# Optimization experiments

Measured on AMD Instinct MI355X. Metric: run time of the kernel, lower is better.

The kernel has to match this reference:

```python
import jax, jax.numpy as jnp
import numpy as np

DIM = 256
NUM_HEADS = 8
WH, WW = 7, 7
N = WH * WW
HEAD_DIM = DIM // NUM_HEADS
SCALE = HEAD_DIM ** -0.5
B_ = 4096
NW = 64  # windows per image


def _relative_position_index():
    # Swin relative position index: (N, N) int32 in [0, (2Wh-1)*(2Ww-1))
    coords = np.stack(np.meshgrid(np.arange(WH), np.arange(WW), indexing='ij'))  # (2, Wh, Ww)
    cf = coords.reshape(2, -1)  # (2, N)
    rel = cf[:, :, None] - cf[:, None, :]  # (2, N, N)
    rel = rel.transpose(1, 2, 0).copy()
    rel[:, :, 0] += WH - 1
    rel[:, :, 1] += WW - 1
    rel[:, :, 0] *= 2 * WW - 1
    return jnp.asarray(rel.sum(-1), dtype=jnp.int32)  # (N, N)


def setup_inputs() -> dict:
    key = jax.random.key(0)
    ks = jax.random.split(key, 7)
    x = jax.random.normal(ks[0], (B_, N, DIM), dtype=jnp.float32)
    mask = jax.random.normal(ks[1], (NW, N, N), dtype=jnp.float32)
    qkv_w = jax.random.normal(ks[2], (3 * DIM, DIM), dtype=jnp.float32) * 0.02
    qkv_b = jnp.zeros((3 * DIM,), dtype=jnp.float32)
    proj_w = jax.random.normal(ks[3], (DIM, DIM), dtype=jnp.float32) * 0.02
    proj_b = jnp.zeros((DIM,), dtype=jnp.float32)
    bias_table = jax.random.normal(ks[4], ((2 * WH - 1) * (2 * WW - 1), NUM_HEADS), dtype=jnp.float32) * 0.02
    rel_index = _relative_position_index()
    return {"x": x, "mask": mask, "qkv_w": qkv_w, "qkv_b": qkv_b,
            "proj_w": proj_w, "proj_b": proj_b, "bias_table": bias_table,
            "rel_index": rel_index}


def reference(x, mask, qkv_w, qkv_b, proj_w, proj_b, bias_table, rel_index):
    Bw, n, c = x.shape
    # qkv projection: (B_, N, 3C) -> (3, B_, nH, N, hd)
    qkv = (x @ qkv_w.T + qkv_b).reshape(Bw, n, 3, NUM_HEADS, HEAD_DIM)
    qkv = qkv.transpose(2, 0, 3, 1, 4)
    q, k, v = qkv[0], qkv[1], qkv[2]
    attn = jnp.einsum('bhqd,bhkd->bhqk', q * SCALE, k)  # (B_, nH, N, N)
    # gathered relative position bias: (nH, N, N)
    rpb = bias_table[rel_index.reshape(-1)].reshape(n, n, NUM_HEADS).transpose(2, 0, 1)
    attn = attn + rpb[None]
    # window mask: reshape batch into (B, nW) and broadcast mask per-window
    nW = mask.shape[0]
    attn = attn.reshape(Bw // nW, nW, NUM_HEADS, n, n) + mask[None, :, None]
    attn = attn.reshape(Bw, NUM_HEADS, n, n)
    attn = jax.nn.softmax(attn, axis=-1)
    out = jnp.einsum('bhqk,bhkd->bhqd', attn, v)  # (B_, nH, N, hd)
    out = out.transpose(0, 2, 1, 3).reshape(Bw, n, c)
    return out @ proj_w.T + proj_b
```

## Files before the change

kernel.cpp:

```cpp
#include <hip/hip_runtime.h>
#include <hip/hip_bf16.h>

typedef __bf16 bf16;
typedef __bf16 bf16x4v __attribute__((ext_vector_type(4)));
typedef __bf16 bf16x8 __attribute__((ext_vector_type(8)));
typedef float  f32x4  __attribute__((ext_vector_type(4)));
typedef float  f32x8  __attribute__((ext_vector_type(8)));

#define MFMA16(A,B,C) __builtin_amdgcn_mfma_f32_16x16x32_bf16((A),(B),(C),0,0,0)

constexpr int   N_TOK = 49;
constexpr int   DIM_C = 256;
constexpr float SCALE = 0.17677669529663687f;

constexpr int SMEM_ELEMS = N_TOK * 256;

constexpr size_t CB_BYTES    = 64ull * 8 * 64 * 64 * 4;
constexpr int    QKVW_ELEMS  = 768 * 256;
constexpr int    PROJW_ELEMS = 256 * 256;

__global__ __launch_bounds__(256) void build_cb_kernel(
    const float* __restrict__ bias_table, const float* __restrict__ mask,
    const int* __restrict__ rel_index, float* __restrict__ cb) {
  int idx = blockIdx.x * 256 + threadIdx.x;
  int j = idx & 63, m = (idx >> 6) & 63, h = (idx >> 12) & 7, w = idx >> 15;
  float v = 0.f;
  if (j < N_TOK && m < N_TOK)
    v = bias_table[rel_index[m * 49 + j] * 8 + h] + mask[(w * 49 + m) * 49 + j];
  cb[idx] = v;
}

__global__ __launch_bounds__(256) void cvt_w_kernel(
    const float* __restrict__ qkv_w, const float* __restrict__ proj_w,
    bf16* __restrict__ qkv_wb, bf16* __restrict__ proj_wb) {
  int i = blockIdx.x * 256 + threadIdx.x;
  if (i < QKVW_ELEMS) qkv_wb[i] = (bf16)qkv_w[i];
  else                proj_wb[i - QKVW_ELEMS] = (bf16)proj_w[i - QKVW_ELEMS];
}

__device__ __forceinline__ bf16x8 repack8(f32x4 Ta, f32x4 Tb, int l15, int lgp) {
  const int s0 = l15 + ((lgp & 1) << 5);
  const bool hi = (lgp & 2) != 0;
  bf16x8 F;
#pragma unroll
  for (int r = 0; r < 4; ++r) {
    float a0 = __shfl(Ta[r], s0);
    float b0 = __shfl(Tb[r], s0);
    F[r] = (bf16)(hi ? b0 : a0);
    float a1 = __shfl(Ta[r], s0 + 16);
    float b1 = __shfl(Tb[r], s0 + 16);
    F[r + 4] = (bf16)(hi ? b1 : a1);
  }
  return F;
}

__device__ __forceinline__ bf16x8 tile_read(const bf16* sm, int mt, int l15, int kk) {
  int m = mt * 16 + l15;
  int mc = m < N_TOK ? m : 48;
  return *reinterpret_cast<const bf16x8*>(&sm[mc * 256 + (kk ^ ((mc & 7) << 3))]);
}

__global__ __launch_bounds__(512, 4) void win_attn_kernel(
    const float* __restrict__ x, const bf16* __restrict__ qkv_wb,
    const float* __restrict__ qkv_b, const bf16* __restrict__ proj_wb,
    const float* __restrict__ proj_b, const float* __restrict__ cb,
    float* __restrict__ out) {
  __shared__ bf16 smem[SMEM_ELEMS];

  const int beta  = blockIdx.x;
  const int w_idx = beta >> 6;
  const int img   = beta & 63;
  const int b     = img * 64 + w_idx;
  const int tid   = threadIdx.x;
  const int wv    = tid >> 6;
  const int l     = tid & 63;
  const int l15   = l & 15, lgp = l >> 4;
  const int h     = wv;

  const f32x4 fzero = {0.f, 0.f, 0.f, 0.f};

  const float* xg = x + (size_t)b * (N_TOK * DIM_C);
  for (int c = tid; c < (N_TOK * DIM_C / 8); c += 512) {
    int m = c >> 5, k0 = (c & 31) * 8;
    f32x8 f = *reinterpret_cast<const f32x8*>(xg + m * 256 + k0);
    bf16x8 v;
#pragma unroll
    for (int e = 0; e < 8; ++e) v[e] = (bf16)f[e];
    *reinterpret_cast<bf16x8*>(&smem[m * 256 + (k0 ^ ((m & 7) << 3))]) = v;
  }
  __syncthreads();

  bf16x8 Qf[4], Kf[4];
  {
    f32x4 dq[2][4], dk[2][4];
#pragma unroll
    for (int i = 0; i < 2; ++i)
      for (int mt = 0; mt < 4; ++mt) { dq[i][mt] = fzero; dk[i][mt] = fzero; }
#pragma unroll 2
    for (int k0 = 0; k0 < 8; ++k0) {
      const int kk = k0 * 32 + lgp * 8;
      bf16x8 X[4];
#pragma unroll
      for (int mt = 0; mt < 4; ++mt) X[mt] = tile_read(smem, mt, l15, kk);
#pragma unroll
      for (int i = 0; i < 2; ++i) {
        int cq = (2 * h + i) * 16 + l15;
        bf16x8 Aq = *reinterpret_cast<const bf16x8*>(qkv_wb + cq * DIM_C + kk);
#pragma unroll
        for (int mt = 0; mt < 4; ++mt) dq[i][mt] = MFMA16(Aq, X[mt], dq[i][mt]);
        int ck = (16 + 2 * h + i) * 16 + l15;
        bf16x8 Ak = *reinterpret_cast<const bf16x8*>(qkv_wb + ck * DIM_C + kk);
#pragma unroll
        for (int mt = 0; mt < 4; ++mt) dk[i][mt] = MFMA16(Ak, X[mt], dk[i][mt]);
      }
    }
#pragma unroll
    for (int i = 0; i < 2; ++i) {
      f32x4 qb = *reinterpret_cast<const f32x4*>(qkv_b + (2 * h + i) * 16 + lgp * 4);
      f32x4 kb = *reinterpret_cast<const f32x4*>(qkv_b + 256 + (2 * h + i) * 16 + lgp * 4);
#pragma unroll
      for (int mt = 0; mt < 4; ++mt)
#pragma unroll
        for (int r = 0; r < 4; ++r) {
          dq[i][mt][r] = (dq[i][mt][r] + qb[r]) * SCALE;
          dk[i][mt][r] += kb[r];
        }
    }
#pragma unroll
    for (int mt = 0; mt < 4; ++mt) Qf[mt] = repack8(dq[0][mt], dq[1][mt], l15, lgp);
#pragma unroll
    for (int jt = 0; jt < 4; ++jt) Kf[jt] = repack8(dk[0][jt], dk[1][jt], l15, lgp);
  }

  bf16x8 Vf[2][2];
  {
    f32x4 dv[2][4];
#pragma unroll
    for (int i = 0; i < 2; ++i)
      for (int mt = 0; mt < 4; ++mt) dv[i][mt] = fzero;
#pragma unroll 2
    for (int k0 = 0; k0 < 8; ++k0) {
      const int kk = k0 * 32 + lgp * 8;
      bf16x8 X[4];
#pragma unroll
      for (int mt = 0; mt < 4; ++mt) X[mt] = tile_read(smem, mt, l15, kk);
#pragma unroll
      for (int i = 0; i < 2; ++i) {
        int cv = (32 + 2 * h + i) * 16 + l15;
        bf16x8 Bw = *reinterpret_cast<const bf16x8*>(qkv_wb + cv * DIM_C + kk);
#pragma unroll
        for (int mt = 0; mt < 4; ++mt) dv[i][mt] = MFMA16(X[mt], Bw, dv[i][mt]);
      }
    }
    __syncthreads();
#pragma unroll
    for (int i = 0; i < 2; ++i) {
      float vb = qkv_b[512 + (32 + 2 * h + i) * 16 + l15 - 512];
#pragma unroll
      for (int mt = 0; mt < 4; ++mt)
#pragma unroll
        for (int r = 0; r < 4; ++r) dv[i][mt][r] += vb;
#pragma unroll
      for (int ks = 0; ks < 2; ++ks)
        Vf[i][ks] = repack8(dv[i][ks * 2], dv[i][ks * 2 + 1], l15, lgp);
    }
  }

  const float* cbp = cb + ((size_t)(w_idx * 8 + h)) * 4096;
#pragma unroll
  for (int mt = 0; mt < 4; ++mt) {
    int mrow = mt * 16 + l15;
    f32x4 cb4[4];
#pragma unroll
    for (int jt = 0; jt < 4; ++jt)
      cb4[jt] = *reinterpret_cast<const f32x4*>(cbp + mrow * 64 + jt * 16 + lgp * 4);
    f32x4 e4[4];
#pragma unroll
    for (int jt = 0; jt < 4; ++jt) e4[jt] = MFMA16(Kf[jt], Qf[mt], fzero);
#pragma unroll
    for (int jt = 0; jt < 4; ++jt)
#pragma unroll
      for (int r = 0; r < 4; ++r) {
        float v = e4[jt][r] + cb4[jt][r];
        if (jt == 3) {
          if (r != 0 || lgp != 0) v = -3.0e38f;
        }
        e4[jt][r] = v;
      }
    float mx = e4[0][0];
#pragma unroll
    for (int jt = 0; jt < 4; ++jt)
#pragma unroll
      for (int r = 0; r < 4; ++r) mx = fmaxf(mx, e4[jt][r]);
    mx = fmaxf(mx, __shfl_xor(mx, 16));
    mx = fmaxf(mx, __shfl_xor(mx, 32));
    float sum = 0.f;
#pragma unroll
    for (int jt = 0; jt < 4; ++jt)
#pragma unroll
      for (int r = 0; r < 4; ++r) {
        float ex = __expf(e4[jt][r] - mx);
        e4[jt][r] = ex;
        sum += ex;
      }
    sum += __shfl_xor(sum, 16);
    sum += __shfl_xor(sum, 32);
    float rinv = 1.0f / sum;

    bf16x8 Pf0 = repack8(e4[0], e4[1], l15, lgp);
    bf16x8 Pf1 = repack8(e4[2], e4[3], l15, lgp);
    f32x4 pv0 = MFMA16(Vf[0][0], Pf0, fzero);
    pv0 = MFMA16(Vf[0][1], Pf1, pv0);
    f32x4 pv1 = MFMA16(Vf[1][0], Pf0, fzero);
    pv1 = MFMA16(Vf[1][1], Pf1, pv1);

    if (mrow < N_TOK) {
      bf16x4v w0, w1;
#pragma unroll
      for (int r = 0; r < 4; ++r) {
        w0[r] = (bf16)(pv0[r] * rinv);
        w1[r] = (bf16)(pv1[r] * rinv);
      }
      int sw = (mrow & 7) << 3;
      int c0 = 32 * h + lgp * 4;
      *reinterpret_cast<bf16x4v*>(&smem[mrow * 256 + (c0 ^ sw)]) = w0;
      *reinterpret_cast<bf16x4v*>(&smem[mrow * 256 + ((c0 + 16) ^ sw)]) = w1;
    }
  }
  __syncthreads();

  f32x4 acc2[2][4];
#pragma unroll
  for (int ci = 0; ci < 2; ++ci)
    for (int mt = 0; mt < 4; ++mt) acc2[ci][mt] = fzero;
#pragma unroll 2
  for (int k0 = 0; k0 < 8; ++k0) {
    const int kk = k0 * 32 + lgp * 8;
    bf16x8 Bao[4];
#pragma unroll
    for (int mt = 0; mt < 4; ++mt) Bao[mt] = tile_read(smem, mt, l15, kk);
#pragma unroll
    for (int ci = 0; ci < 2; ++ci) {
      int c = (2 * wv + ci) * 16 + l15;
      bf16x8 Aw = *reinterpret_cast<const bf16x8*>(proj_wb + c * DIM_C + kk);
#pragma unroll
      for (int mt = 0; mt < 4; ++mt) acc2[ci][mt] = MFMA16(Aw, Bao[mt], acc2[ci][mt]);
    }
  }
  float* ob = out + (size_t)b * (N_TOK * DIM_C);
#pragma unroll
  for (int ci = 0; ci < 2; ++ci) {
    int c0 = (2 * wv + ci) * 16 + lgp * 4;
    f32x4 pb = *reinterpret_cast<const f32x4*>(proj_b + c0);
#pragma unroll
    for (int mt = 0; mt < 4; ++mt) {
      int mrow = mt * 16 + l15;
      if (mrow < N_TOK) {
        f32x4 o;
#pragma unroll
        for (int r = 0; r < 4; ++r) o[r] = acc2[ci][mt][r] + pb[r];
        *reinterpret_cast<f32x4*>(ob + mrow * 256 + c0) = o;
      }
    }
  }
}

extern "C" void kernel_launch(void* const* d_in, const int* in_sizes, int n_in,
                              void* d_out, int out_size, void* d_ws, size_t ws_size,
                              hipStream_t stream) {
  const float* x          = (const float*)d_in[0];
  const float* mask       = (const float*)d_in[1];
  const float* qkv_w      = (const float*)d_in[2];
  const float* qkv_b      = (const float*)d_in[3];
  const float* proj_w     = (const float*)d_in[4];
  const float* proj_b     = (const float*)d_in[5];
  const float* bias_table = (const float*)d_in[6];
  const int*   rel_index  = (const int*)d_in[7];

  float* cb      = (float*)d_ws;
  bf16*  qkv_wb  = (bf16*)((char*)d_ws + CB_BYTES);
  bf16*  proj_wb = (bf16*)((char*)d_ws + CB_BYTES + QKVW_ELEMS * 2);

  hipLaunchKernelGGL(build_cb_kernel, dim3(8192), dim3(256), 0, stream,
                     bias_table, mask, rel_index, cb);
  hipLaunchKernelGGL(cvt_w_kernel, dim3(1024), dim3(256), 0, stream,
                     qkv_w, proj_w, qkv_wb, proj_wb);
  hipLaunchKernelGGL(win_attn_kernel, dim3(4096), dim3(512), 0, stream,
                     x, qkv_wb, qkv_b, proj_wb, proj_b, cb, (float*)d_out);
}
```

Before: 511.2 us.

## Split fused window attention into QKV GEMM, attention, and projection GEMM kernels

Replaces the single fused per-window kernel with three kernels: a tiled 128x128 QKV GEMM over all tokens that writes bf16 Q/K/V to workspace in head-major layout, a per-(window,head) attention kernel, and a tiled projection GEMM. The goal is better weight reuse and MFMA utilization from large GEMM tiles than the per-window fused version, which re-read weights for each window. In exchange it adds large intermediate round trips through global memory (Q/K/V and attention output, on the order of a hundred MB each way) and two extra launches, plus scattered 2-byte stores in the QKV epilogue.

After: 435.4 us. 14.8% less time.

```diff
diff --git a/kernel.cpp b/kernel.cpp
--- a/kernel.cpp
+++ b/kernel.cpp
@@ -2,22 +2,19 @@
 #include <hip/hip_bf16.h>
 
 typedef __bf16 bf16;
-typedef __bf16 bf16x4v __attribute__((ext_vector_type(4)));
 typedef __bf16 bf16x8 __attribute__((ext_vector_type(8)));
 typedef float  f32x4  __attribute__((ext_vector_type(4)));
-typedef float  f32x8  __attribute__((ext_vector_type(8)));
 
 #define MFMA16(A,B,C) __builtin_amdgcn_mfma_f32_16x16x32_bf16((A),(B),(C),0,0,0)
 
-constexpr int   N_TOK = 49;
-constexpr int   DIM_C = 256;
 constexpr float SCALE = 0.17677669529663687f;
 
-constexpr int SMEM_ELEMS = N_TOK * 256;
-
-constexpr size_t CB_BYTES    = 64ull * 8 * 64 * 64 * 4;
-constexpr int    QKVW_ELEMS  = 768 * 256;
-constexpr int    PROJW_ELEMS = 256 * 256;
+constexpr size_t CB_OFF    = 0;
+constexpr size_t QKVW_OFF  = 8388608;
+constexpr size_t PROJW_OFF = QKVW_OFF + 768*256*2;
+constexpr size_t QI_OFF    = PROJW_OFF + 256*256*2;
+constexpr size_t TEN_ELEMS = 51380224ull;
+constexpr size_t AO_OFF    = QI_OFF + 3*TEN_ELEMS*2;
 
 __global__ __launch_bounds__(256) void build_cb_kernel(
     const float* __restrict__ bias_table, const float* __restrict__ mask,
@@ -25,7 +22,7 @@
   int idx = blockIdx.x * 256 + threadIdx.x;
   int j = idx & 63, m = (idx >> 6) & 63, h = (idx >> 12) & 7, w = idx >> 15;
   float v = 0.f;
-  if (j < N_TOK && m < N_TOK)
+  if (j < 49 && m < 49)
     v = bias_table[rel_index[m * 49 + j] * 8 + h] + mask[(w * 49 + m) * 49 + j];
   cb[idx] = v;
 }
@@ -34,8 +31,96 @@
     const float* __restrict__ qkv_w, const float* __restrict__ proj_w,
     bf16* __restrict__ qkv_wb, bf16* __restrict__ proj_wb) {
   int i = blockIdx.x * 256 + threadIdx.x;
-  if (i < QKVW_ELEMS) qkv_wb[i] = (bf16)qkv_w[i];
-  else                proj_wb[i - QKVW_ELEMS] = (bf16)proj_w[i - QKVW_ELEMS];
+  if (i < 768 * 256) qkv_wb[i] = (bf16)qkv_w[i];
+  else               proj_wb[i - 768 * 256] = (bf16)proj_w[i - 768 * 256];
+}
+
+__device__ __forceinline__ bf16x8 frag(const bf16* S, int row, int kchunk) {
+  return *reinterpret_cast<const bf16x8*>(&S[row * 64 + ((kchunk ^ (row & 7)) * 8)]);
+}
+
+__global__ __launch_bounds__(256) void gemm_qkv_kernel(
+    const float* __restrict__ x, const bf16* __restrict__ qkv_wb,
+    const float* __restrict__ qkv_b, bf16* __restrict__ qkv_i) {
+  __shared__ __align__(16) bf16 As[128 * 64];
+  __shared__ __align__(16) bf16 Bs[128 * 64];
+  const int bid = blockIdx.x;
+  const int xcd = bid & 7, idx = bid >> 3;
+  const int m_t = xcd * 196 + idx / 6;
+  const int n_t = idx % 6;
+  const int tid = threadIdx.x;
+  const int wv = tid >> 6, l = tid & 63, l15 = l & 15, lgp = l >> 4;
+  const int wr = wv >> 1, wc = wv & 1;
+
+  const f32x4 fzero = {0.f, 0.f, 0.f, 0.f};
+  f32x4 acc[4][4];
+#pragma unroll
+  for (int mt = 0; mt < 4; ++mt)
+#pragma unroll
+    for (int nt = 0; nt < 4; ++nt) acc[mt][nt] = fzero;
+
+  for (int ks = 0; ks < 4; ++ks) {
+    const int k0 = ks * 64;
+#pragma unroll
+    for (int i = 0; i < 4; ++i) {
+      int c = i * 256 + tid;
+      int row = c >> 3, kc = c & 7;
+      const float* src = x + (size_t)(m_t * 128 + row) * 256 + k0 + kc * 8;
+      f32x4 f0 = *reinterpret_cast<const f32x4*>(src);
+      f32x4 f1 = *reinterpret_cast<const f32x4*>(src + 4);
+      bf16x8 v8;
+#pragma unroll
+      for (int e = 0; e < 4; ++e) { v8[e] = (bf16)f0[e]; v8[e + 4] = (bf16)f1[e]; }
+      *reinterpret_cast<bf16x8*>(&As[row * 64 + ((kc ^ (row & 7)) * 8)]) = v8;
+    }
+#pragma unroll
+    for (int i = 0; i < 4; ++i) {
+      int c = i * 256 + tid;
+      int row = c >> 3, kc = c & 7;
+      bf16x8 w8 = *reinterpret_cast<const bf16x8*>(
+          qkv_wb + (size_t)(n_t * 128 + row) * 256 + k0 + kc * 8);
+      *reinterpret_cast<bf16x8*>(&Bs[row * 64 + ((kc ^ (row & 7)) * 8)]) = w8;
+    }
+    __syncthreads();
+#pragma unroll
+    for (int kk = 0; kk < 2; ++kk) {
+      bf16x8 Af[4], Bf[4];
+#pragma unroll
+      for (int mt = 0; mt < 4; ++mt) Af[mt] = frag(As, wr * 64 + mt * 16 + l15, kk * 4 + lgp);
+#pragma unroll
+      for (int nt = 0; nt < 4; ++nt) Bf[nt] = frag(Bs, wc * 64 + nt * 16 + l15, kk * 4 + lgp);
+#pragma unroll
+      for (int mt = 0; mt < 4; ++mt)
+#pragma unroll
+        for (int nt = 0; nt < 4; ++nt) acc[mt][nt] = MFMA16(Af[mt], Bf[nt], acc[mt][nt]);
+    }
+    __syncthreads();
+  }
+
+  const int tsel = n_t >> 1;
+  bf16* tb = qkv_i + (size_t)tsel * TEN_ELEMS;
+  const float sc = (tsel == 0) ? SCALE : 1.0f;
+  float bias[4]; int hh[4], dd[4];
+#pragma unroll
+  for (int nt = 0; nt < 4; ++nt) {
+    int n_g = n_t * 128 + wc * 64 + nt * 16 + l15;
+    bias[nt] = qkv_b[n_g];
+    int nl = n_g & 255;
+    hh[nt] = nl >> 5; dd[nt] = nl & 31;
+  }
+#pragma unroll
+  for (int mt = 0; mt < 4; ++mt) {
+#pragma unroll
+    for (int r = 0; r < 4; ++r) {
+      int r_g = m_t * 128 + wr * 64 + mt * 16 + lgp * 4 + r;
+      int b = r_g / 49, m = r_g - b * 49;
+#pragma unroll
+      for (int nt = 0; nt < 4; ++nt) {
+        tb[((size_t)(b * 8 + hh[nt]) * 49 + m) * 32 + dd[nt]] =
+            (bf16)((acc[mt][nt][r] + bias[nt]) * sc);
+      }
+    }
+  }
 }
 
 __device__ __forceinline__ bf16x8 repack8(f32x4 Ta, f32x4 Tb, int l15, int lgp) {
@@ -54,139 +139,76 @@
   return F;
 }
 
-__device__ __forceinline__ bf16x8 tile_read(const bf16* sm, int mt, int l15, int kk) {
-  int m = mt * 16 + l15;
-  int mc = m < N_TOK ? m : 48;
-  return *reinterpret_cast<const bf16x8*>(&sm[mc * 256 + (kk ^ ((mc & 7) << 3))]);
-}
-
-__global__ __launch_bounds__(512, 4) void win_attn_kernel(
-    const float* __restrict__ x, const bf16* __restrict__ qkv_wb,
-    const float* __restrict__ qkv_b, const bf16* __restrict__ proj_wb,
-    const float* __restrict__ proj_b, const float* __restrict__ cb,
-    float* __restrict__ out) {
-  __shared__ bf16 smem[SMEM_ELEMS];
-
-  const int beta  = blockIdx.x;
-  const int w_idx = beta >> 6;
-  const int img   = beta & 63;
-  const int b     = img * 64 + w_idx;
-  const int tid   = threadIdx.x;
-  const int wv    = tid >> 6;
-  const int l     = tid & 63;
-  const int l15   = l & 15, lgp = l >> 4;
-  const int h     = wv;
-
+__global__ __launch_bounds__(256) void attn_kernel(
+    const bf16* __restrict__ qkv_i, const float* __restrict__ cb,
+    bf16* __restrict__ ao) {
+  __shared__ __align__(16) bf16 Vs[4][64 * 32];
+  const int tid = threadIdx.x, wv = tid >> 6, l = tid & 63;
+  const int l15 = l & 15, lgp = l >> 4;
+  const int g = blockIdx.x * 4 + wv;
+  const int b = g >> 3, h = g & 7;
+
+  const bf16* qp = qkv_i + (size_t)(b * 8 + h) * 1568;
+  const bf16* kp = qp + TEN_ELEMS;
+  const bf16* vp = kp + TEN_ELEMS;
+  bf16* vsm = &Vs[wv][0];
+
+#pragma unroll
+  for (int i = 0; i < 4; ++i) {
+    int c = i * 64 + l;
+    if (c < 196)
+      *reinterpret_cast<bf16x8*>(&vsm[c * 8]) =
+          *reinterpret_cast<const bf16x8*>(vp + c * 8);
+  }
+  {
+    const bf16x8 z8 = {(bf16)0.f,(bf16)0.f,(bf16)0.f,(bf16)0.f,
+                       (bf16)0.f,(bf16)0.f,(bf16)0.f,(bf16)0.f};
+    if (l < 60) *reinterpret_cast<bf16x8*>(&vsm[1568 + l * 8]) = z8;
+  }
+  __syncthreads();
+
+  bf16x8 Qf[4], Kf[4];
+#pragma unroll
+  for (int mt = 0; mt < 4; ++mt) {
+    int m = mt * 16 + l15; int mc = m < 49 ? m : 48;
+    Qf[mt] = *reinterpret_cast<const bf16x8*>(qp + mc * 32 + lgp * 8);
+  }
+#pragma unroll
+  for (int jt = 0; jt < 4; ++jt) {
+    int j = jt * 16 + l15; int jc = j < 49 ? j : 48;
+    Kf[jt] = *reinterpret_cast<const bf16x8*>(kp + jc * 32 + lgp * 8);
+  }
+  bf16x8 Vb[2][2];
+#pragma unroll
+  for (int dt = 0; dt < 2; ++dt)
+#pragma unroll
+    for (int ksx = 0; ksx < 2; ++ksx) {
+#pragma unroll
+      for (int u = 0; u < 8; ++u) {
+        int j = ksx * 32 + lgp * 8 + u;
+        Vb[dt][ksx][u] = vsm[j * 32 + dt * 16 + l15];
+      }
+    }
+
+  const float* cbp = cb + (size_t)((b & 63) * 8 + h) * 4096;
+  bf16* aob = ao + (size_t)b * 12544;
   const f32x4 fzero = {0.f, 0.f, 0.f, 0.f};
 
-  const float* xg = x + (size_t)b * (N_TOK * DIM_C);
-  for (int c = tid; c < (N_TOK * DIM_C / 8); c += 512) {
-    int m = c >> 5, k0 = (c & 31) * 8;
-    f32x8 f = *reinterpret_cast<const f32x8*>(xg + m * 256 + k0);
-    bf16x8 v;
-#pragma unroll
-    for (int e = 0; e < 8; ++e) v[e] = (bf16)f[e];
-    *reinterpret_cast<bf16x8*>(&smem[m * 256 + (k0 ^ ((m & 7) << 3))]) = v;
-  }
-  __syncthreads();
-
-  bf16x8 Qf[4], Kf[4];
-  {
-    f32x4 dq[2][4], dk[2][4];
-#pragma unroll
-    for (int i = 0; i < 2; ++i)
-      for (int mt = 0; mt < 4; ++mt) { dq[i][mt] = fzero; dk[i][mt] = fzero; }
-#pragma unroll 2
-    for (int k0 = 0; k0 < 8; ++k0) {
-      const int kk = k0 * 32 + lgp * 8;
-      bf16x8 X[4];
-#pragma unroll
-      for (int mt = 0; mt < 4; ++mt) X[mt] = tile_read(smem, mt, l15, kk);
-#pragma unroll
-      for (int i = 0; i < 2; ++i) {
-        int cq = (2 * h + i) * 16 + l15;
-        bf16x8 Aq = *reinterpret_cast<const bf16x8*>(qkv_wb + cq * DIM_C + kk);
-#pragma unroll
-        for (int mt = 0; mt < 4; ++mt) dq[i][mt] = MFMA16(Aq, X[mt], dq[i][mt]);
-        int ck = (16 + 2 * h + i) * 16 + l15;
-        bf16x8 Ak = *reinterpret_cast<const bf16x8*>(qkv_wb + ck * DIM_C + kk);
-#pragma unroll
-        for (int mt = 0; mt < 4; ++mt) dk[i][mt] = MFMA16(Ak, X[mt], dk[i][mt]);
-      }
-    }
-#pragma unroll
-    for (int i = 0; i < 2; ++i) {
-      f32x4 qb = *reinterpret_cast<const f32x4*>(qkv_b + (2 * h + i) * 16 + lgp * 4);
-      f32x4 kb = *reinterpret_cast<const f32x4*>(qkv_b + 256 + (2 * h + i) * 16 + lgp * 4);
-#pragma unroll
-      for (int mt = 0; mt < 4; ++mt)
-#pragma unroll
-        for (int r = 0; r < 4; ++r) {
-          dq[i][mt][r] = (dq[i][mt][r] + qb[r]) * SCALE;
-          dk[i][mt][r] += kb[r];
-        }
-    }
-#pragma unroll
-    for (int mt = 0; mt < 4; ++mt) Qf[mt] = repack8(dq[0][mt], dq[1][mt], l15, lgp);
-#pragma unroll
-    for (int jt = 0; jt < 4; ++jt) Kf[jt] = repack8(dk[0][jt], dk[1][jt], l15, lgp);
-  }
-
-  bf16x8 Vf[2][2];
-  {
-    f32x4 dv[2][4];
-#pragma unroll
-    for (int i = 0; i < 2; ++i)
-      for (int mt = 0; mt < 4; ++mt) dv[i][mt] = fzero;
-#pragma unroll 2
-    for (int k0 = 0; k0 < 8; ++k0) {
-      const int kk = k0 * 32 + lgp * 8;
-      bf16x8 X[4];
-#pragma unroll
-      for (int mt = 0; mt < 4; ++mt) X[mt] = tile_read(smem, mt, l15, kk);
-#pragma unroll
-      for (int i = 0; i < 2; ++i) {
-        int cv = (32 + 2 * h + i) * 16 + l15;
-        bf16x8 Bw = *reinterpret_cast<const bf16x8*>(qkv_wb + cv * DIM_C + kk);
-#pragma unroll
-        for (int mt = 0; mt < 4; ++mt) dv[i][mt] = MFMA16(X[mt], Bw, dv[i][mt]);
-      }
-    }
-    __syncthreads();
-#pragma unroll
-    for (int i = 0; i < 2; ++i) {
-      float vb = qkv_b[512 + (32 + 2 * h + i) * 16 + l15 - 512];
-#pragma unroll
-      for (int mt = 0; mt < 4; ++mt)
-#pragma unroll
-        for (int r = 0; r < 4; ++r) dv[i][mt][r] += vb;
-#pragma unroll
-      for (int ks = 0; ks < 2; ++ks)
-        Vf[i][ks] = repack8(dv[i][ks * 2], dv[i][ks * 2 + 1], l15, lgp);
-    }
-  }
-
-  const float* cbp = cb + ((size_t)(w_idx * 8 + h)) * 4096;
 #pragma unroll
   for (int mt = 0; mt < 4; ++mt) {
     int mrow = mt * 16 + l15;
-    f32x4 cb4[4];
-#pragma unroll
-    for (int jt = 0; jt < 4; ++jt)
-      cb4[jt] = *reinterpret_cast<const f32x4*>(cbp + mrow * 64 + jt * 16 + lgp * 4);
     f32x4 e4[4];
 #pragma unroll
     for (int jt = 0; jt < 4; ++jt) e4[jt] = MFMA16(Kf[jt], Qf[mt], fzero);
 #pragma unroll
-    for (int jt = 0; jt < 4; ++jt)
-#pragma unroll
-      for (int r = 0; r < 4; ++r) {
-        float v = e4[jt][r] + cb4[jt][r];
-        if (jt == 3) {
-          if (r != 0 || lgp != 0) v = -3.0e38f;
-        }
-        e4[jt][r] = v;
-      }
+    for (int jt = 0; jt < 4; ++jt) {
+      f32x4 c4 = *reinterpret_cast<const f32x4*>(cbp + mrow * 64 + jt * 16 + lgp * 4);
+#pragma unroll
+      for (int r = 0; r < 4; ++r) e4[jt][r] += c4[r];
+    }
+    if (lgp != 0) { e4[3][0] = -3.0e38f; }
+    e4[3][1] = -3.0e38f; e4[3][2] = -3.0e38f; e4[3][3] = -3.0e38f;
+
     float mx = e4[0][0];
 #pragma unroll
     for (int jt = 0; jt < 4; ++jt)
@@ -206,61 +228,94 @@
     sum += __shfl_xor(sum, 16);
     sum += __shfl_xor(sum, 32);
     float rinv = 1.0f / sum;
+#pragma unroll
+    for (int jt = 0; jt < 4; ++jt)
+#pragma unroll
+      for (int r = 0; r < 4; ++r) e4[jt][r] *= rinv;
 
     bf16x8 Pf0 = repack8(e4[0], e4[1], l15, lgp);
     bf16x8 Pf1 = repack8(e4[2], e4[3], l15, lgp);
-    f32x4 pv0 = MFMA16(Vf[0][0], Pf0, fzero);
-    pv0 = MFMA16(Vf[0][1], Pf1, pv0);
-    f32x4 pv1 = MFMA16(Vf[1][0], Pf0, fzero);
-    pv1 = MFMA16(Vf[1][1], Pf1, pv1);
-
-    if (mrow < N_TOK) {
-      bf16x4v w0, w1;
-#pragma unroll
-      for (int r = 0; r < 4; ++r) {
-        w0[r] = (bf16)(pv0[r] * rinv);
-        w1[r] = (bf16)(pv1[r] * rinv);
+    f32x4 pv[2];
+#pragma unroll
+    for (int dt = 0; dt < 2; ++dt) {
+      pv[dt] = MFMA16(Pf0, Vb[dt][0], fzero);
+      pv[dt] = MFMA16(Pf1, Vb[dt][1], pv[dt]);
+    }
+#pragma unroll
+    for (int r = 0; r < 4; ++r) {
+      int m_g = mt * 16 + lgp * 4 + r;
+      if (m_g < 49) {
+#pragma unroll
+        for (int dt = 0; dt < 2; ++dt)
+          aob[m_g * 256 + h * 32 + dt * 16 + l15] = (bf16)pv[dt][r];
       }
-      int sw = (mrow & 7) << 3;
-      int c0 = 32 * h + lgp * 4;
-      *reinterpret_cast<bf16x4v*>(&smem[mrow * 256 + (c0 ^ sw)]) = w0;
-      *reinterpret_cast<bf16x4v*>(&smem[mrow * 256 + ((c0 + 16) ^ sw)]) = w1;
-    }
-  }
-  __syncthreads();
-
-  f32x4 acc2[2][4];
-#pragma unroll
-  for (int ci = 0; ci < 2; ++ci)
-    for (int mt = 0; mt < 4; ++mt) acc2[ci][mt] = fzero;
-#pragma unroll 2
-  for (int k0 = 0; k0 < 8; ++k0) {
-    const int kk = k0 * 32 + lgp * 8;
-    bf16x8 Bao[4];
-#pragma unroll
-    for (int mt = 0; mt < 4; ++mt) Bao[mt] = tile_read(smem, mt, l15, kk);
-#pragma unroll
-    for (int ci = 0; ci < 2; ++ci) {
-      int c = (2 * wv + ci) * 16 + l15;
-      bf16x8 Aw = *reinterpret_cast<const bf16x8*>(proj_wb + c * DIM_C + kk);
-#pragma unroll
-      for (int mt = 0; mt < 4; ++mt) acc2[ci][mt] = MFMA16(Aw, Bao[mt], acc2[ci][mt]);
-    }
-  }
-  float* ob = out + (size_t)b * (N_TOK * DIM_C);
-#pragma unroll
-  for (int ci = 0; ci < 2; ++ci) {
-    int c0 = (2 * wv + ci) * 16 + lgp * 4;
-    f32x4 pb = *reinterpret_cast<const f32x4*>(proj_b + c0);
-#pragma unroll
-    for (int mt = 0; mt < 4; ++mt) {
-      int mrow = mt * 16 + l15;
-      if (mrow < N_TOK) {
-        f32x4 o;
-#pragma unroll
-        for (int r = 0; r < 4; ++r) o[r] = acc2[ci][mt][r] + pb[r];
-        *reinterpret_cast<f32x4*>(ob + mrow * 256 + c0) = o;
-      }
+    }
+  }
+}
+
+__global__ __launch_bounds__(256) void gemm_proj_kernel(
+    const bf16* __restrict__ ao, const bf16* __restrict__ proj_wb,
+    const float* __restrict__ proj_b, float* __restrict__ out) {
+  __shared__ __align__(16) bf16 As[128 * 64];
+  __shared__ __align__(16) bf16 Bs[128 * 64];
+  const int bid = blockIdx.x;
+  const int xcd = bid & 7, idx = bid >> 3;
+  const int m_t = xcd * 196 + idx / 2;
+  const int n_t = idx % 2;
+  const int tid = threadIdx.x;
+  const int wv = tid >> 6, l = tid & 63, l15 = l & 15, lgp = l >> 4;
+  const int wr = wv >> 1, wc = wv & 1;
+
+  const f32x4 fzero = {0.f, 0.f, 0.f, 0.f};
+  f32x4 acc[4][4];
+#pragma unroll
+  for (int mt = 0; mt < 4; ++mt)
+#pragma unroll
+    for (int nt = 0; nt < 4; ++nt) acc[mt][nt] = fzero;
+
+  for (int ks = 0; ks < 4; ++ks) {
+    const int k0 = ks * 64;
+#pragma unroll
+    for (int i = 0; i < 4; ++i) {
+      int c = i * 256 + tid;
+      int row = c >> 3, kc = c & 7;
+      bf16x8 a8 = *reinterpret_cast<const bf16x8*>(
+          ao + (size_t)(m_t * 128 + row) * 256 + k0 + kc * 8);
+      *reinterpret_cast<bf16x8*>(&As[row * 64 + ((kc ^ (row & 7)) * 8)]) = a8;
+      bf16x8 w8 = *reinterpret_cast<const bf16x8*>(
+          proj_wb + (size_t)(n_t * 128 + row) * 256 + k0 + kc * 8);
+      *reinterpret_cast<bf16x8*>(&Bs[row * 64 + ((kc ^ (row & 7)) * 8)]) = w8;
+    }
+    __syncthreads();
+#pragma unroll
+    for (int kk = 0; kk < 2; ++kk) {
+      bf16x8 Af[4], Bf[4];
+#pragma unroll
+      for (int mt = 0; mt < 4; ++mt) Af[mt] = frag(As, wr * 64 + mt * 16 + l15, kk * 4 + lgp);
+#pragma unroll
+      for (int nt = 0; nt < 4; ++nt) Bf[nt] = frag(Bs, wc * 64 + nt * 16 + l15, kk * 4 + lgp);
+#pragma unroll
+      for (int mt = 0; mt < 4; ++mt)
+#pragma unroll
+        for (int nt = 0; nt < 4; ++nt) acc[mt][nt] = MFMA16(Af[mt], Bf[nt], acc[mt][nt]);
+    }
+    __syncthreads();
+  }
+
+  float bias[4]; int cg[4];
+#pragma unroll
+  for (int nt = 0; nt < 4; ++nt) {
+    cg[nt] = n_t * 128 + wc * 64 + nt * 16 + l15;
+    bias[nt] = proj_b[cg[nt]];
+  }
+#pragma unroll
+  for (int mt = 0; mt < 4; ++mt) {
+#pragma unroll
+    for (int r = 0; r < 4; ++r) {
+      size_t r_g = (size_t)(m_t * 128 + wr * 64 + mt * 16 + lgp * 4 + r);
+#pragma unroll
+      for (int nt = 0; nt < 4; ++nt)
+        out[r_g * 256 + cg[nt]] = acc[mt][nt][r] + bias[nt];
     }
   }
 }
@@ -277,14 +332,21 @@
   const float* bias_table = (const float*)d_in[6];
   const int*   rel_index  = (const int*)d_in[7];
 
-  float* cb      = (float*)d_ws;
-  bf16*  qkv_wb  = (bf16*)((char*)d_ws + CB_BYTES);
-  bf16*  proj_wb = (bf16*)((char*)d_ws + CB_BYTES + QKVW_ELEMS * 2);
+  char* ws = (char*)d_ws;
+  float* cb      = (float*)(ws + CB_OFF);
+  bf16*  qkv_wb  = (bf16*)(ws + QKVW_OFF);
+  bf16*  proj_wb = (bf16*)(ws + PROJW_OFF);
+  bf16*  qkv_i   = (bf16*)(ws + QI_OFF);
+  bf16*  ao      = (bf16*)(ws + AO_OFF);
 
   hipLaunchKernelGGL(build_cb_kernel, dim3(8192), dim3(256), 0, stream,
                      bias_table, mask, rel_index, cb);
   hipLaunchKernelGGL(cvt_w_kernel, dim3(1024), dim3(256), 0, stream,
                      qkv_w, proj_w, qkv_wb, proj_wb);
-  hipLaunchKernelGGL(win_attn_kernel, dim3(4096), dim3(512), 0, stream,
-                     x, qkv_wb, qkv_b, proj_wb, proj_b, cb, (float*)d_out);
-}
+  hipLaunchKernelGGL(gemm_qkv_kernel, dim3(9408), dim3(256), 0, stream,
+                     x, qkv_wb, qkv_b, qkv_i);
+  hipLaunchKernelGGL(attn_kernel, dim3(8192), dim3(256), 0, stream,
+                     qkv_i, cb, ao);
+  hipLaunchKernelGGL(gemm_proj_kernel, dim3(3136), dim3(256), 0, stream,
+                     ao, proj_wb, proj_b, (float*)d_out);
+}
```
